# Kernel optimization log

Measured on AMD Instinct MI355X. Metric: run time of the kernel, lower is better.

The kernel has to match this reference:

```python
import jax, jax.numpy as jnp
import numpy as np

DIM = 256
NUM_HEADS = 4
HEAD_DIM = DIM // NUM_HEADS
SCALE = HEAD_DIM ** -0.5
LN_EPS = 1e-5


def setup_inputs() -> dict:
    key = jax.random.key(0)
    ks = jax.random.split(key, 12)
    V, B, C, H, W = 3, 2, DIM, 32, 32
    s = 0.02
    return {
        "features": jax.random.normal(ks[0], (V, B, C, H, W), jnp.float32),
        "Wq": jax.random.normal(ks[1], (DIM, DIM), jnp.float32) * s,
        "bq": jnp.zeros((DIM,), jnp.float32),
        "Wk": jax.random.normal(ks[2], (DIM, DIM), jnp.float32) * s,
        "bk": jnp.zeros((DIM,), jnp.float32),
        "Wv": jax.random.normal(ks[3], (DIM, DIM), jnp.float32) * s,
        "bv": jnp.zeros((DIM,), jnp.float32),
        "Wp": jax.random.normal(ks[4], (DIM, DIM), jnp.float32) * s,
        "bp": jnp.zeros((DIM,), jnp.float32),
        "gamma": jnp.ones((DIM,), jnp.float32),
        "beta": jnp.zeros((DIM,), jnp.float32),
    }


def reference(features, Wq, bq, Wk, bk, Wv, bv, Wp, bp, gamma, beta):
    V, B, C, H, W = features.shape
    N = H * W
    L = V * N
    # concat views along token axis: [B, V*N, C]
    x = features.reshape(V, B, C, N).transpose(1, 0, 3, 2).reshape(B, L, C)
    # QKV projections (torch Linear: x @ W.T + b)
    q = (x @ Wq.T + bq).reshape(B, L, NUM_HEADS, HEAD_DIM).transpose(0, 2, 1, 3)
    k = (x @ Wk.T + bk).reshape(B, L, NUM_HEADS, HEAD_DIM).transpose(0, 2, 1, 3)
    v = (x @ Wv.T + bv).reshape(B, L, NUM_HEADS, HEAD_DIM).transpose(0, 2, 1, 3)
    # full attention (chunked loop in original is exact, dropout off in eval)
    attn = jax.nn.softmax(jnp.einsum('bhqd,bhkd->bhqk', q, k) * SCALE, axis=-1)
    o = jnp.einsum('bhqk,bhkd->bhqd', attn, v)  # [B, H, L, D]
    o = o.transpose(0, 2, 1, 3).reshape(B, L, C)
    # output proj + LayerNorm
    o = o @ Wp.T + bp
    mu = jnp.mean(o, axis=-1, keepdims=True)
    var = jnp.mean(jnp.square(o - mu), axis=-1, keepdims=True)
    o = (o - mu) * jax.lax.rsqrt(var + LN_EPS) * gamma + beta
    # mean over views, back to [B, C, H, W]
    o = o.reshape(B, V, N, C).mean(axis=1)
    return o.reshape(B, H, W, C).transpose(0, 3, 1, 2)
```

## Files before the change

### kernel.cpp

```cpp
#include <hip/hip_runtime.h>
#include <hip/hip_bf16.h>

#define V_ 3
#define B_ 2
#define C_ 256
#define N_ 1024
#define L_ 3072
#define NH 4
#define DH 64
#define SCALE 0.125f
#define LOG2E 1.44269504088896340736f

typedef __attribute__((ext_vector_type(8))) short short8;
typedef __attribute__((ext_vector_type(4))) float floatx4;
typedef unsigned short u16;
typedef unsigned int u32;

__device__ __forceinline__ u16 f2bf(float f) {
    union { float f; u32 u; } c; c.f = f;
    u32 u = c.u;
    u32 lsb = (u >> 16) & 1u;
    u += 0x7fffu + lsb;
    return (u16)(u >> 16);
}
__device__ __forceinline__ u32 pk_bf16(float a, float b) {
    __hip_bfloat162 h = __float22bfloat162_rn(make_float2(a, b));
    union { __hip_bfloat162 h; u32 u; } cv; cv.h = h; return cv.u;
}

__global__ __launch_bounds__(256) void k_prep_gather(
    const float* __restrict__ feat,
    const float* __restrict__ Wq, const float* __restrict__ Wk,
    const float* __restrict__ Wv, const float* __restrict__ Wp,
    u16* __restrict__ x, u16* __restrict__ Wb) {
    int bid = blockIdx.x;
    int t = threadIdx.x;
    if (bid < 384) {
        __shared__ u16 tile[64][66];
        int n0 = (bid & 15) << 6;
        int c0 = ((bid >> 4) & 3) << 6;
        int b  = (bid >> 6) & 1;
        int v  = bid >> 7;
        const float* src = feat + ((size_t)((v * B_ + b) * C_ + c0)) * N_ + n0;
        for (int i = 0; i < 8; ++i) {
            int idx = i * 256 + t;
            int cl = idx >> 5;
            int np2 = idx & 31;
            float2 f = *(const float2*)(src + (size_t)cl * N_ + np2 * 2);
            *(u32*)&tile[cl][np2 * 2] = pk_bf16(f.x, f.y);
        }
        __syncthreads();
        u16* dst = x + ((size_t)(b * L_ + v * N_ + n0)) * C_ + c0;
        for (int i = 0; i < 8; ++i) {
            int idx = i * 256 + t;
            int nl = idx >> 5;
            int cl = (idx & 31) * 2;
            u32 uu = (u32)tile[cl][nl] | ((u32)tile[cl + 1][nl] << 16);
            *(u32*)(dst + (size_t)nl * C_ + cl) = uu;
        }
    } else {
        int idx = (bid - 384) * 256 + t;
        int g0 = idx * 16;
        int m = g0 >> 16;
        const float* src = (m == 0) ? Wq : (m == 1) ? Wk : (m == 2) ? Wv : Wp;
        int off = g0 & 65535;
#pragma unroll
        for (int e = 0; e < 8; ++e) {
            float2 f = *(const float2*)(src + off + e * 2);
            ((u32*)(Wb + g0))[e] = pk_bf16(f.x, f.y);
        }
    }
}


__global__ __launch_bounds__(64) void k_qkv(
    const u16* __restrict__ x, const u16* __restrict__ Wb,
    const float* __restrict__ bq, const float* __restrict__ bk,
    const float* __restrict__ bv,
    u16* __restrict__ Qf, u16* __restrict__ Kf, u16* __restrict__ Vf) {
    int bid = blockIdx.x;
    int npc = bid & 3;
    int rest = bid >> 2;
    int m  = rest / 192;
    int rb = rest % 192;
    int b  = rb / 96;
    int r0 = (rb % 96) * 32;
    int lane = threadIdx.x;
    int quad = lane >> 4, m16 = lane & 15;

    const u16* xrow0 = x + ((size_t)(b * L_ + r0 + m16)) * C_ + quad * 8;
    const u16* xrow1 = xrow0 + (size_t)16 * C_;
    short8 a0[8], a1[8];
#pragma unroll
    for (int kc = 0; kc < 8; ++kc) {
        a0[kc] = *(const short8*)(xrow0 + kc * 32);
        a1[kc] = *(const short8*)(xrow1 + kc * 32);
    }

    const u16* W   = Wb + (size_t)m * 65536;
    const float* bs = (m == 0) ? bq : (m == 1) ? bk : bv;
    float scale = (m == 0) ? (SCALE * LOG2E) : 1.0f;

#pragma unroll
    for (int np = npc * 2; np < npc * 2 + 2; ++np) {
        int nt0 = np * 2;
        const u16* w0 = W + (size_t)(nt0 * 16 + m16) * C_ + quad * 8;
        const u16* w1 = w0 + 16 * C_;
        short8 wf0[8], wf1[8];
#pragma unroll
        for (int kc = 0; kc < 8; ++kc) {
            wf0[kc] = *(const short8*)(w0 + kc * 32);
            wf1[kc] = *(const short8*)(w1 + kc * 32);
        }
        floatx4 acc00 = {0.f,0.f,0.f,0.f}, acc01 = {0.f,0.f,0.f,0.f};
        floatx4 acc10 = {0.f,0.f,0.f,0.f}, acc11 = {0.f,0.f,0.f,0.f};
#pragma unroll
        for (int kc = 0; kc < 8; ++kc) {
            acc00 = __builtin_amdgcn_mfma_f32_16x16x32_bf16(a0[kc], wf0[kc], acc00, 0, 0, 0);
            acc01 = __builtin_amdgcn_mfma_f32_16x16x32_bf16(a0[kc], wf1[kc], acc01, 0, 0, 0);
            acc10 = __builtin_amdgcn_mfma_f32_16x16x32_bf16(a1[kc], wf0[kc], acc10, 0, 0, 0);
            acc11 = __builtin_amdgcn_mfma_f32_16x16x32_bf16(a1[kc], wf1[kc], acc11, 0, 0, 0);
        }
#pragma unroll
        for (int gi = 0; gi < 2; ++gi)
#pragma unroll
        for (int half = 0; half < 2; ++half) {
            int dout = (nt0 + half) * 16 + m16;
            float bias = bs[dout];
            int h = dout >> 6, dh = dout & 63;
            size_t bh = (size_t)(b * NH + h);
            floatx4 acc = gi ? (half ? acc11 : acc10) : (half ? acc01 : acc00);
            float f0 = (acc[0] + bias) * scale, f1 = (acc[1] + bias) * scale;
            float f2 = (acc[2] + bias) * scale, f3 = (acc[3] + bias) * scale;
            int lr0 = r0 + gi * 16 + quad * 4;
            if (m == 2) {
                int tile = lr0 >> 6, kk = lr0 & 63;
                int halfv = kk >> 5, quadp = (kk >> 3) & 3, j0 = kk & 7;
                int ntv = dh >> 4, m16pp = dh & 15;
                u32* p = (u32*)(Vf + (bh * 48 + tile) * 4096 +
                                ((size_t)((ntv * 2 + halfv) * 64 + quadp * 16 + m16pp)) * 8 + j0);
                p[0] = pk_bf16(f0, f1);
                p[1] = pk_bf16(f2, f3);
            } else {
                int cc = dh >> 5, quadp = (dh >> 3) & 3, j = dh & 7;
                u32 p01 = pk_bf16(f0, f1);
                u32 p23 = pk_bf16(f2, f3);
                if (m == 0) {
#pragma unroll
                    for (int r = 0; r < 4; ++r) {
                        int lr = lr0 + r;
                        int grp = lr >> 4, m16p = lr & 15;
                        u32 pk = (r < 2) ? p01 : p23;
                        u16 val = (r & 1) ? (u16)(pk >> 16) : (u16)pk;
                        Qf[(bh * 192 + grp) * 1024 +
                           (size_t)(cc * 64 + quadp * 16 + m16p) * 8 + j] = val;
                    }
                } else {
#pragma unroll
                    for (int r = 0; r < 4; ++r) {
                        int lr = lr0 + r;
                        int tile = lr >> 6, rr = lr & 63;
                        int ntk = rr >> 4, m16p = rr & 15;
                        u32 pk = (r < 2) ? p01 : p23;
                        u16 val = (r & 1) ? (u16)(pk >> 16) : (u16)pk;
                        Kf[(bh * 48 + tile) * 4096 +
                           (size_t)((ntk * 2 + cc) * 64 + quadp * 16 + m16p) * 8 + j] = val;
                    }
                }
            }
        }
    }
}

__global__ __launch_bounds__(256, 2) void k_attn(
    const u16* __restrict__ Qf, const u16* __restrict__ Kf,
    const u16* __restrict__ Vf, u16* __restrict__ o) {
    __shared__ __align__(16) char smem[36864];
    __shared__ float l_red[3][3][16];
    u16* PL = (u16*)smem;
    float* o_red = (float*)smem;
    int bid = blockIdx.x;
    int qt = bid & 63;
    int h  = (bid >> 6) & 3;
    int b  = bid >> 8;
    int lane = threadIdx.x & 63;
    int w    = threadIdx.x >> 6;
    int quad = lane >> 4, m16 = lane & 15;
    int q0 = qt * 48;
    size_t bh = (size_t)(b * NH + h);

    const u16* qbase = Qf + (bh * 192 + qt * 3) * 1024 + (size_t)lane * 8;
    const u16* kbase = Kf + bh * 48 * 4096 + (size_t)lane * 8;
    const u16* vbase = Vf + bh * 48 * 4096 + (size_t)lane * 8;

    short8 aq[3][2];
#pragma unroll
    for (int g = 0; g < 3; ++g) {
        aq[g][0] = *(const short8*)(qbase + g * 1024);
        aq[g][1] = *(const short8*)(qbase + g * 1024 + 512);
    }

    float l_s[3] = {0.f, 0.f, 0.f};
    floatx4 o_acc[3][4];
#pragma unroll
    for (int g = 0; g < 3; ++g)
#pragma unroll
        for (int nt = 0; nt < 4; ++nt) o_acc[g][nt] = (floatx4){0.f, 0.f, 0.f, 0.f};

    int kt0 = w * 12;
    short8 kb[8], vb[8];
#pragma unroll
    for (int f = 0; f < 8; ++f)
        kb[f] = *(const short8*)(kbase + (size_t)kt0 * 4096 + f * 512);

    for (int i = 0; i < 12; ++i) {
        size_t tbase = (size_t)(kt0 + i) * 4096;
#pragma unroll
        for (int f = 0; f < 8; ++f)
            vb[f] = *(const short8*)(vbase + tbase + f * 512);
#pragma unroll
        for (int g = 0; g < 3; ++g) {
            floatx4 s[4];
#pragma unroll
            for (int nt = 0; nt < 4; ++nt) {
                floatx4 z = {0.f, 0.f, 0.f, 0.f};
                z = __builtin_amdgcn_mfma_f32_16x16x32_bf16(kb[nt * 2], aq[g][0], z, 0, 0, 0);
                s[nt] = __builtin_amdgcn_mfma_f32_16x16x32_bf16(kb[nt * 2 + 1], aq[g][1], z, 0, 0, 0);
            }
            u16* plrow = PL + (((w * 3 + g) * 16) + m16) * 72;
            float lsum = 0.f;
#pragma unroll
            for (int nt = 0; nt < 4; ++nt) {
                float p0 = __builtin_amdgcn_exp2f(s[nt][0]);
                float p1 = __builtin_amdgcn_exp2f(s[nt][1]);
                float p2 = __builtin_amdgcn_exp2f(s[nt][2]);
                float p3 = __builtin_amdgcn_exp2f(s[nt][3]);
                lsum += (p0 + p1) + (p2 + p3);
                uint2 pk; pk.x = pk_bf16(p0, p1); pk.y = pk_bf16(p2, p3);
                *(uint2*)(plrow + nt * 16 + quad * 4) = pk;
            }
            l_s[g] += lsum;
            short8 bp0 = *(const short8*)(plrow + quad * 8);
            short8 bp1 = *(const short8*)(plrow + 32 + quad * 8);
#pragma unroll
            for (int nt = 0; nt < 4; ++nt) {
                o_acc[g][nt] = __builtin_amdgcn_mfma_f32_16x16x32_bf16(vb[nt * 2], bp0, o_acc[g][nt], 0, 0, 0);
                o_acc[g][nt] = __builtin_amdgcn_mfma_f32_16x16x32_bf16(vb[nt * 2 + 1], bp1, o_acc[g][nt], 0, 0, 0);
            }
        }
        if (i < 11) {
#pragma unroll
            for (int f = 0; f < 8; ++f)
                kb[f] = *(const short8*)(kbase + tbase + 4096 + f * 512);
        }
    }
    float l_row[3];
#pragma unroll
    for (int g = 0; g < 3; ++g) {
        float ps = l_s[g];
        ps += __shfl_xor(ps, 16);
        ps += __shfl_xor(ps, 32);
        l_row[g] = ps;
    }
    __syncthreads();
    if (w > 0) {
#pragma unroll
        for (int g = 0; g < 3; ++g) {
#pragma unroll
            for (int nt = 0; nt < 4; ++nt)
                *(floatx4*)&o_red[(((w - 1) * 3 + g) * 4 + nt) * 256 + lane * 4] = o_acc[g][nt];
            if (quad == 0) l_red[w - 1][g][m16] = l_row[g];
        }
    }
    __syncthreads();
    if (w == 0) {
#pragma unroll
        for (int g = 0; g < 3; ++g) {
            float lt = __builtin_amdgcn_rcpf(
                l_row[g] + l_red[0][g][m16] + l_red[1][g][m16] + l_red[2][g][m16]);
#pragma unroll
            for (int nt = 0; nt < 4; ++nt) {
                floatx4 tot = o_acc[g][nt];
#pragma unroll
                for (int w1 = 0; w1 < 3; ++w1)
                    tot += *(const floatx4*)&o_red[((w1 * 3 + g) * 4 + nt) * 256 + lane * 4];
                uint2 pk;
                pk.x = pk_bf16(tot[0] * lt, tot[1] * lt);
                pk.y = pk_bf16(tot[2] * lt, tot[3] * lt);
                *(uint2*)(o + ((size_t)(b * L_ + q0 + g * 16 + m16)) * C_ +
                          h * 64 + nt * 16 + quad * 4) = pk;
            }
        }
    }
}

__global__ __launch_bounds__(256) void k_proj_ln(
    const u16* __restrict__ o, const u16* __restrict__ Wpb,
    const float* __restrict__ bp,
    const float* __restrict__ gamma, const float* __restrict__ beta,
    u16* __restrict__ oln) {
    __shared__ float sred[4][16];
    __shared__ float sred2[4][16];
    int bid = blockIdx.x;
    int n0 = (bid & 63) << 4;
    int b  = (bid >> 6) & 1;
    int v  = bid >> 7;
    int lane = threadIdx.x & 63;
    int w    = threadIdx.x >> 6;
    int quad = lane >> 4, m16 = lane & 15;

    const u16* orow = o + ((size_t)(b * L_ + v * N_ + n0 + m16)) * C_ + quad * 8;
    short8 a[8];
#pragma unroll
    for (int kc = 0; kc < 8; ++kc) a[kc] = *(const short8*)(orow + kc * 32);

    float pr[4][4];
#pragma unroll
    for (int j = 0; j < 4; ++j) {
        int nt = w * 4 + j;
        const u16* wrow = Wpb + (size_t)(nt * 16 + m16) * C_ + quad * 8;
        floatx4 acc = {0.f, 0.f, 0.f, 0.f};
#pragma unroll
        for (int kc = 0; kc < 8; ++kc) {
            short8 bfr = *(const short8*)(wrow + kc * 32);
            acc = __builtin_amdgcn_mfma_f32_16x16x32_bf16(a[kc], bfr, acc, 0, 0, 0);
        }
        float bias = bp[nt * 16 + m16];
#pragma unroll
        for (int r = 0; r < 4; ++r) pr[j][r] = acc[r] + bias;
    }
#pragma unroll
    for (int r = 0; r < 4; ++r) {
        float sm = pr[0][r] + pr[1][r] + pr[2][r] + pr[3][r];
        sm += __shfl_xor(sm, 1); sm += __shfl_xor(sm, 2);
        sm += __shfl_xor(sm, 4); sm += __shfl_xor(sm, 8);
        if (m16 == 0) sred[w][quad * 4 + r] = sm;
    }
    __syncthreads();
    float mu[4];
#pragma unroll
    for (int r = 0; r < 4; ++r) {
        int row = quad * 4 + r;
        mu[r] = (sred[0][row] + sred[1][row] + sred[2][row] + sred[3][row]) * (1.0f / C_);
    }
#pragma unroll
    for (int r = 0; r < 4; ++r) {
        float sq = 0.f;
#pragma unroll
        for (int j = 0; j < 4; ++j) { float d = pr[j][r] - mu[r]; sq += d * d; }
        sq += __shfl_xor(sq, 1); sq += __shfl_xor(sq, 2);
        sq += __shfl_xor(sq, 4); sq += __shfl_xor(sq, 8);
        if (m16 == 0) sred2[w][quad * 4 + r] = sq;
    }
    __syncthreads();
    float rs[4];
#pragma unroll
    for (int r = 0; r < 4; ++r) {
        int row = quad * 4 + r;
        float var = (sred2[0][row] + sred2[1][row] + sred2[2][row] + sred2[3][row]) * (1.0f / C_);
        rs[r] = __builtin_amdgcn_rsqf(var + 1e-5f);
    }
#pragma unroll
    for (int j = 0; j < 4; ++j) {
        int nt = w * 4 + j;
        int c = nt * 16 + m16;
        float g  = gamma[c];
        float be = beta[c];
#pragma unroll
        for (int r = 0; r < 4; ++r) {
            int row = quad * 4 + r;
            oln[((size_t)((v * B_ + b) * N_ + n0 + row)) * C_ + c] =
                f2bf((pr[j][r] - mu[r]) * rs[r] * g + be);
        }
    }
}

__global__ __launch_bounds__(256) void k_mean_t(
    const u16* __restrict__ oln, float* __restrict__ out) {
    __shared__ float tile[64][65];
    int bid = blockIdx.x;
    int n0 = (bid & 15) << 6;
    int c0 = ((bid >> 4) & 3) << 6;
    int b  = bid >> 6;
    int t = threadIdx.x;
    union { u32 u; float f; } cv;
    for (int i = 0; i < 16; ++i) {
        int idx = i * 256 + t;
        int nl = idx >> 6, cl = idx & 63;
        float sm = 0.f;
#pragma unroll
        for (int v = 0; v < 3; ++v) {
            u16 raw = oln[((size_t)((v * B_ + b) * N_ + n0 + nl)) * C_ + c0 + cl];
            cv.u = ((u32)raw) << 16;
            sm += cv.f;
        }
        tile[cl][nl] = sm * (1.0f / 3.0f);
    }
    __syncthreads();
    for (int i = 0; i < 16; ++i) {
        int idx = i * 256 + t;
        int cl = idx >> 6, nl = idx & 63;
        out[((size_t)(b * C_ + c0 + cl)) * N_ + n0 + nl] = tile[cl][nl];
    }
}

extern "C" void kernel_launch(void* const* d_in, const int* in_sizes, int n_in,
                              void* d_out, int out_size, void* d_ws, size_t ws_size,
                              hipStream_t stream) {
    (void)in_sizes; (void)n_in; (void)out_size; (void)ws_size;
    const float* feat  = (const float*)d_in[0];
    const float* Wq    = (const float*)d_in[1];
    const float* bq    = (const float*)d_in[2];
    const float* Wk    = (const float*)d_in[3];
    const float* bk    = (const float*)d_in[4];
    const float* Wv    = (const float*)d_in[5];
    const float* bv    = (const float*)d_in[6];
    const float* Wp    = (const float*)d_in[7];
    const float* bp    = (const float*)d_in[8];
    const float* gamma = (const float*)d_in[9];
    const float* beta  = (const float*)d_in[10];
    float* out = (float*)d_out;

    size_t SZ = (size_t)B_ * L_ * C_;
    u16* x   = (u16*)d_ws;
    u16* Qf  = x + SZ;
    u16* Kf  = Qf + SZ;
    u16* Vf  = Kf + SZ;
    u16* o   = Vf + SZ;
    u16* Wb  = o + SZ;
    u16* oln = Wb + 4 * 65536;

    k_prep_gather<<<dim3(448), dim3(256), 0, stream>>>(feat, Wq, Wk, Wv, Wp, x, Wb);
    k_qkv<<<dim3(2304), dim3(64), 0, stream>>>(x, Wb, bq, bk, bv, Qf, Kf, Vf);
    k_attn<<<dim3(512), dim3(256), 0, stream>>>(Qf, Kf, Vf, o);
    k_proj_ln<<<dim3(384), dim3(256), 0, stream>>>(o, Wb + 3 * 65536, bp, gamma, beta, oln);
    k_mean_t<<<dim3(128), dim3(256), 0, stream>>>(oln, out);
}
```

Measured before the change: 134.3 us.

## Split attention keys across two blocks, vectorize QKV and LN epilogue stores

The attention kernel is split along the key dimension into two halves, doubling the grid to 1024 blocks. Each block writes unnormalized fp32 partial outputs and row sums, and a new combine kernel adds them and normalizes. K and V fragments now share one register array to cut register pressure, and launch bounds target 3 blocks per CU. The Q/K projection and the proj+LayerNorm kernel swap MFMA operand order so each lane holds 4 consecutive channels, allowing vectorized bias loads and 8-byte stores instead of scattered 2-byte stores. The cost is an extra launch plus fp32 partial-result traffic.

```diff
diff --git a/kernel.cpp b/kernel.cpp
--- a/kernel.cpp
+++ b/kernel.cpp
@@ -72,7 +72,6 @@
     }
 }
 
-
 __global__ __launch_bounds__(64) void k_qkv(
     const u16* __restrict__ x, const u16* __restrict__ Wb,
     const float* __restrict__ bq, const float* __restrict__ bk,
@@ -96,44 +95,41 @@
         a0[kc] = *(const short8*)(xrow0 + kc * 32);
         a1[kc] = *(const short8*)(xrow1 + kc * 32);
     }
-
-    const u16* W   = Wb + (size_t)m * 65536;
-    const float* bs = (m == 0) ? bq : (m == 1) ? bk : bv;
-    float scale = (m == 0) ? (SCALE * LOG2E) : 1.0f;
-
-#pragma unroll
-    for (int np = npc * 2; np < npc * 2 + 2; ++np) {
-        int nt0 = np * 2;
-        const u16* w0 = W + (size_t)(nt0 * 16 + m16) * C_ + quad * 8;
-        const u16* w1 = w0 + 16 * C_;
-        short8 wf0[8], wf1[8];
-#pragma unroll
-        for (int kc = 0; kc < 8; ++kc) {
-            wf0[kc] = *(const short8*)(w0 + kc * 32);
-            wf1[kc] = *(const short8*)(w1 + kc * 32);
-        }
-        floatx4 acc00 = {0.f,0.f,0.f,0.f}, acc01 = {0.f,0.f,0.f,0.f};
-        floatx4 acc10 = {0.f,0.f,0.f,0.f}, acc11 = {0.f,0.f,0.f,0.f};
-#pragma unroll
-        for (int kc = 0; kc < 8; ++kc) {
-            acc00 = __builtin_amdgcn_mfma_f32_16x16x32_bf16(a0[kc], wf0[kc], acc00, 0, 0, 0);
-            acc01 = __builtin_amdgcn_mfma_f32_16x16x32_bf16(a0[kc], wf1[kc], acc01, 0, 0, 0);
-            acc10 = __builtin_amdgcn_mfma_f32_16x16x32_bf16(a1[kc], wf0[kc], acc10, 0, 0, 0);
-            acc11 = __builtin_amdgcn_mfma_f32_16x16x32_bf16(a1[kc], wf1[kc], acc11, 0, 0, 0);
-        }
-#pragma unroll
-        for (int gi = 0; gi < 2; ++gi)
-#pragma unroll
-        for (int half = 0; half < 2; ++half) {
-            int dout = (nt0 + half) * 16 + m16;
-            float bias = bs[dout];
-            int h = dout >> 6, dh = dout & 63;
-            size_t bh = (size_t)(b * NH + h);
-            floatx4 acc = gi ? (half ? acc11 : acc10) : (half ? acc01 : acc00);
-            float f0 = (acc[0] + bias) * scale, f1 = (acc[1] + bias) * scale;
-            float f2 = (acc[2] + bias) * scale, f3 = (acc[3] + bias) * scale;
-            int lr0 = r0 + gi * 16 + quad * 4;
-            if (m == 2) {
+    const u16* W = Wb + (size_t)m * 65536;
+
+    if (m == 2) {
+#pragma unroll
+        for (int np = npc * 2; np < npc * 2 + 2; ++np) {
+            int nt0 = np * 2;
+            const u16* w0 = W + (size_t)(nt0 * 16 + m16) * C_ + quad * 8;
+            const u16* w1 = w0 + 16 * C_;
+            short8 wf0[8], wf1[8];
+#pragma unroll
+            for (int kc = 0; kc < 8; ++kc) {
+                wf0[kc] = *(const short8*)(w0 + kc * 32);
+                wf1[kc] = *(const short8*)(w1 + kc * 32);
+            }
+            floatx4 acc00 = {0.f,0.f,0.f,0.f}, acc01 = {0.f,0.f,0.f,0.f};
+            floatx4 acc10 = {0.f,0.f,0.f,0.f}, acc11 = {0.f,0.f,0.f,0.f};
+#pragma unroll
+            for (int kc = 0; kc < 8; ++kc) {
+                acc00 = __builtin_amdgcn_mfma_f32_16x16x32_bf16(a0[kc], wf0[kc], acc00, 0, 0, 0);
+                acc01 = __builtin_amdgcn_mfma_f32_16x16x32_bf16(a0[kc], wf1[kc], acc01, 0, 0, 0);
+                acc10 = __builtin_amdgcn_mfma_f32_16x16x32_bf16(a1[kc], wf0[kc], acc10, 0, 0, 0);
+                acc11 = __builtin_amdgcn_mfma_f32_16x16x32_bf16(a1[kc], wf1[kc], acc11, 0, 0, 0);
+            }
+#pragma unroll
+            for (int gi = 0; gi < 2; ++gi)
+#pragma unroll
+            for (int half = 0; half < 2; ++half) {
+                int dout = (nt0 + half) * 16 + m16;
+                float bias = bv[dout];
+                int h = dout >> 6, dh = dout & 63;
+                size_t bh = (size_t)(b * NH + h);
+                floatx4 acc = gi ? (half ? acc11 : acc10) : (half ? acc01 : acc00);
+                float f0 = acc[0] + bias, f1 = acc[1] + bias;
+                float f2 = acc[2] + bias, f3 = acc[3] + bias;
+                int lr0 = r0 + gi * 16 + quad * 4;
                 int tile = lr0 >> 6, kk = lr0 & 63;
                 int halfv = kk >> 5, quadp = (kk >> 3) & 3, j0 = kk & 7;
                 int ntv = dh >> 4, m16pp = dh & 15;
@@ -141,52 +137,79 @@
                                 ((size_t)((ntv * 2 + halfv) * 64 + quadp * 16 + m16pp)) * 8 + j0);
                 p[0] = pk_bf16(f0, f1);
                 p[1] = pk_bf16(f2, f3);
-            } else {
-                int cc = dh >> 5, quadp = (dh >> 3) & 3, j = dh & 7;
-                u32 p01 = pk_bf16(f0, f1);
-                u32 p23 = pk_bf16(f2, f3);
+            }
+        }
+    } else {
+        const float* bs = (m == 0) ? bq : bk;
+        float scale = (m == 0) ? (SCALE * LOG2E) : 1.0f;
+#pragma unroll
+        for (int np = npc * 2; np < npc * 2 + 2; ++np) {
+            int nt0 = np * 2;
+            const u16* w0 = W + (size_t)(nt0 * 16 + m16) * C_ + quad * 8;
+            const u16* w1 = w0 + 16 * C_;
+            short8 wf0[8], wf1[8];
+#pragma unroll
+            for (int kc = 0; kc < 8; ++kc) {
+                wf0[kc] = *(const short8*)(w0 + kc * 32);
+                wf1[kc] = *(const short8*)(w1 + kc * 32);
+            }
+            floatx4 acc00 = {0.f,0.f,0.f,0.f}, acc01 = {0.f,0.f,0.f,0.f};
+            floatx4 acc10 = {0.f,0.f,0.f,0.f}, acc11 = {0.f,0.f,0.f,0.f};
+#pragma unroll
+            for (int kc = 0; kc < 8; ++kc) {
+                acc00 = __builtin_amdgcn_mfma_f32_16x16x32_bf16(wf0[kc], a0[kc], acc00, 0, 0, 0);
+                acc01 = __builtin_amdgcn_mfma_f32_16x16x32_bf16(wf0[kc], a1[kc], acc01, 0, 0, 0);
+                acc10 = __builtin_amdgcn_mfma_f32_16x16x32_bf16(wf1[kc], a0[kc], acc10, 0, 0, 0);
+                acc11 = __builtin_amdgcn_mfma_f32_16x16x32_bf16(wf1[kc], a1[kc], acc11, 0, 0, 0);
+            }
+#pragma unroll
+            for (int tt = 0; tt < 2; ++tt)
+#pragma unroll
+            for (int gi = 0; gi < 2; ++gi) {
+                int ntb = (nt0 + tt) * 16;
+                int h = ntb >> 6;
+                size_t bh = (size_t)(b * NH + h);
+                int dh0 = (ntb & 63) + quad * 4;
+                int cc = dh0 >> 5, qp = (dh0 >> 3) & 3, j0 = dh0 & 7;
+                float4 b4 = *(const float4*)(bs + ntb + quad * 4);
+                floatx4 acc = tt ? (gi ? acc11 : acc10) : (gi ? acc01 : acc00);
+                float f0 = (acc[0] + b4.x) * scale, f1 = (acc[1] + b4.y) * scale;
+                float f2 = (acc[2] + b4.z) * scale, f3 = (acc[3] + b4.w) * scale;
+                uint2 pk;
+                pk.x = pk_bf16(f0, f1);
+                pk.y = pk_bf16(f2, f3);
+                int token = r0 + gi * 16 + m16;
                 if (m == 0) {
-#pragma unroll
-                    for (int r = 0; r < 4; ++r) {
-                        int lr = lr0 + r;
-                        int grp = lr >> 4, m16p = lr & 15;
-                        u32 pk = (r < 2) ? p01 : p23;
-                        u16 val = (r & 1) ? (u16)(pk >> 16) : (u16)pk;
-                        Qf[(bh * 192 + grp) * 1024 +
-                           (size_t)(cc * 64 + quadp * 16 + m16p) * 8 + j] = val;
-                    }
+                    int grp = (r0 >> 4) + gi;
+                    *(uint2*)(Qf + (bh * 192 + grp) * 1024 +
+                              (size_t)(cc * 64 + qp * 16 + m16) * 8 + j0) = pk;
                 } else {
-#pragma unroll
-                    for (int r = 0; r < 4; ++r) {
-                        int lr = lr0 + r;
-                        int tile = lr >> 6, rr = lr & 63;
-                        int ntk = rr >> 4, m16p = rr & 15;
-                        u32 pk = (r < 2) ? p01 : p23;
-                        u16 val = (r & 1) ? (u16)(pk >> 16) : (u16)pk;
-                        Kf[(bh * 48 + tile) * 4096 +
-                           (size_t)((ntk * 2 + cc) * 64 + quadp * 16 + m16p) * 8 + j] = val;
-                    }
+                    int tile = token >> 6;
+                    int ntk = ((r0 & 63) >> 4) + gi;
+                    *(uint2*)(Kf + (bh * 48 + tile) * 4096 +
+                              (size_t)((ntk * 2 + cc) * 64 + qp * 16 + m16) * 8 + j0) = pk;
                 }
             }
         }
     }
 }
 
-__global__ __launch_bounds__(256, 2) void k_attn(
+__global__ __launch_bounds__(256, 3) void k_attn(
     const u16* __restrict__ Qf, const u16* __restrict__ Kf,
-    const u16* __restrict__ Vf, u16* __restrict__ o) {
+    const u16* __restrict__ Vf, float* __restrict__ o_p, float* __restrict__ l_p) {
     __shared__ __align__(16) char smem[36864];
     __shared__ float l_red[3][3][16];
     u16* PL = (u16*)smem;
     float* o_red = (float*)smem;
     int bid = blockIdx.x;
-    int qt = bid & 63;
-    int h  = (bid >> 6) & 3;
-    int b  = bid >> 8;
+    int rest = bid & 511;
+    int s  = bid >> 9;
+    int qt = rest & 63;
+    int h  = (rest >> 6) & 3;
+    int b  = rest >> 8;
     int lane = threadIdx.x & 63;
     int w    = threadIdx.x >> 6;
     int quad = lane >> 4, m16 = lane & 15;
-    int q0 = qt * 48;
     size_t bh = (size_t)(b * NH + h);
 
     const u16* qbase = Qf + (bh * 192 + qt * 3) * 1024 + (size_t)lane * 8;
@@ -207,51 +230,50 @@
 #pragma unroll
         for (int nt = 0; nt < 4; ++nt) o_acc[g][nt] = (floatx4){0.f, 0.f, 0.f, 0.f};
 
-    int kt0 = w * 12;
-    short8 kb[8], vb[8];
-#pragma unroll
-    for (int f = 0; f < 8; ++f)
-        kb[f] = *(const short8*)(kbase + (size_t)kt0 * 4096 + f * 512);
-
-    for (int i = 0; i < 12; ++i) {
+    int kt0 = s * 24 + w * 6;
+    short8 kv[8];
+
+    for (int i = 0; i < 6; ++i) {
         size_t tbase = (size_t)(kt0 + i) * 4096;
 #pragma unroll
         for (int f = 0; f < 8; ++f)
-            vb[f] = *(const short8*)(vbase + tbase + f * 512);
+            kv[f] = *(const short8*)(kbase + tbase + f * 512);
 #pragma unroll
         for (int g = 0; g < 3; ++g) {
-            floatx4 s[4];
+            floatx4 sx[4];
 #pragma unroll
             for (int nt = 0; nt < 4; ++nt) {
                 floatx4 z = {0.f, 0.f, 0.f, 0.f};
-                z = __builtin_amdgcn_mfma_f32_16x16x32_bf16(kb[nt * 2], aq[g][0], z, 0, 0, 0);
-                s[nt] = __builtin_amdgcn_mfma_f32_16x16x32_bf16(kb[nt * 2 + 1], aq[g][1], z, 0, 0, 0);
+                z = __builtin_amdgcn_mfma_f32_16x16x32_bf16(kv[nt * 2], aq[g][0], z, 0, 0, 0);
+                sx[nt] = __builtin_amdgcn_mfma_f32_16x16x32_bf16(kv[nt * 2 + 1], aq[g][1], z, 0, 0, 0);
             }
             u16* plrow = PL + (((w * 3 + g) * 16) + m16) * 72;
             float lsum = 0.f;
 #pragma unroll
             for (int nt = 0; nt < 4; ++nt) {
-                float p0 = __builtin_amdgcn_exp2f(s[nt][0]);
-                float p1 = __builtin_amdgcn_exp2f(s[nt][1]);
-                float p2 = __builtin_amdgcn_exp2f(s[nt][2]);
-                float p3 = __builtin_amdgcn_exp2f(s[nt][3]);
+                float p0 = __builtin_amdgcn_exp2f(sx[nt][0]);
+                float p1 = __builtin_amdgcn_exp2f(sx[nt][1]);
+                float p2 = __builtin_amdgcn_exp2f(sx[nt][2]);
+                float p3 = __builtin_amdgcn_exp2f(sx[nt][3]);
                 lsum += (p0 + p1) + (p2 + p3);
                 uint2 pk; pk.x = pk_bf16(p0, p1); pk.y = pk_bf16(p2, p3);
                 *(uint2*)(plrow + nt * 16 + quad * 4) = pk;
             }
             l_s[g] += lsum;
+        }
+#pragma unroll
+        for (int f = 0; f < 8; ++f)
+            kv[f] = *(const short8*)(vbase + tbase + f * 512);
+#pragma unroll
+        for (int g = 0; g < 3; ++g) {
+            const u16* plrow = PL + (((w * 3 + g) * 16) + m16) * 72;
             short8 bp0 = *(const short8*)(plrow + quad * 8);
             short8 bp1 = *(const short8*)(plrow + 32 + quad * 8);
 #pragma unroll
             for (int nt = 0; nt < 4; ++nt) {
-                o_acc[g][nt] = __builtin_amdgcn_mfma_f32_16x16x32_bf16(vb[nt * 2], bp0, o_acc[g][nt], 0, 0, 0);
-                o_acc[g][nt] = __builtin_amdgcn_mfma_f32_16x16x32_bf16(vb[nt * 2 + 1], bp1, o_acc[g][nt], 0, 0, 0);
-            }
-        }
-        if (i < 11) {
-#pragma unroll
-            for (int f = 0; f < 8; ++f)
-                kb[f] = *(const short8*)(kbase + tbase + 4096 + f * 512);
+                o_acc[g][nt] = __builtin_amdgcn_mfma_f32_16x16x32_bf16(kv[nt * 2], bp0, o_acc[g][nt], 0, 0, 0);
+                o_acc[g][nt] = __builtin_amdgcn_mfma_f32_16x16x32_bf16(kv[nt * 2 + 1], bp1, o_acc[g][nt], 0, 0, 0);
+            }
         }
     }
     float l_row[3];
@@ -276,21 +298,44 @@
     if (w == 0) {
 #pragma unroll
         for (int g = 0; g < 3; ++g) {
-            float lt = __builtin_amdgcn_rcpf(
-                l_row[g] + l_red[0][g][m16] + l_red[1][g][m16] + l_red[2][g][m16]);
+            if (quad == 0)
+                l_p[(size_t)bid * 48 + g * 16 + m16] =
+                    l_row[g] + l_red[0][g][m16] + l_red[1][g][m16] + l_red[2][g][m16];
 #pragma unroll
             for (int nt = 0; nt < 4; ++nt) {
                 floatx4 tot = o_acc[g][nt];
 #pragma unroll
                 for (int w1 = 0; w1 < 3; ++w1)
                     tot += *(const floatx4*)&o_red[((w1 * 3 + g) * 4 + nt) * 256 + lane * 4];
-                uint2 pk;
-                pk.x = pk_bf16(tot[0] * lt, tot[1] * lt);
-                pk.y = pk_bf16(tot[2] * lt, tot[3] * lt);
-                *(uint2*)(o + ((size_t)(b * L_ + q0 + g * 16 + m16)) * C_ +
-                          h * 64 + nt * 16 + quad * 4) = pk;
-            }
-        }
+                *(floatx4*)&o_p[(((size_t)bid * 3 + g) * 4 + nt) * 256 + lane * 4] = tot;
+            }
+        }
+    }
+}
+
+__global__ __launch_bounds__(192) void k_comb(
+    const float* __restrict__ o_p, const float* __restrict__ l_p,
+    u16* __restrict__ o) {
+    int bid = blockIdx.x;
+    int qt = bid & 63;
+    int h  = (bid >> 6) & 3;
+    int b  = bid >> 8;
+    int lane = threadIdx.x & 63;
+    int g    = threadIdx.x >> 6;
+    int quad = lane >> 4, m16 = lane & 15;
+    float l = l_p[(size_t)bid * 48 + g * 16 + m16] +
+              l_p[(size_t)(bid + 512) * 48 + g * 16 + m16];
+    float lt = __builtin_amdgcn_rcpf(l);
+#pragma unroll
+    for (int nt = 0; nt < 4; ++nt) {
+        floatx4 t0 = *(const floatx4*)&o_p[(((size_t)bid * 3 + g) * 4 + nt) * 256 + lane * 4];
+        floatx4 t1 = *(const floatx4*)&o_p[(((size_t)(bid + 512) * 3 + g) * 4 + nt) * 256 + lane * 4];
+        floatx4 tot = t0 + t1;
+        uint2 pk;
+        pk.x = pk_bf16(tot[0] * lt, tot[1] * lt);
+        pk.y = pk_bf16(tot[2] * lt, tot[3] * lt);
+        *(uint2*)(o + ((size_t)(b * L_ + qt * 48 + g * 16 + m16)) * C_ +
+                  h * 64 + nt * 16 + quad * 4) = pk;
     }
 }
 
@@ -323,55 +368,45 @@
 #pragma unroll
         for (int kc = 0; kc < 8; ++kc) {
             short8 bfr = *(const short8*)(wrow + kc * 32);
-            acc = __builtin_amdgcn_mfma_f32_16x16x32_bf16(a[kc], bfr, acc, 0, 0, 0);
-        }
-        float bias = bp[nt * 16 + m16];
-#pragma unroll
-        for (int r = 0; r < 4; ++r) pr[j][r] = acc[r] + bias;
-    }
-#pragma unroll
-    for (int r = 0; r < 4; ++r) {
-        float sm = pr[0][r] + pr[1][r] + pr[2][r] + pr[3][r];
-        sm += __shfl_xor(sm, 1); sm += __shfl_xor(sm, 2);
-        sm += __shfl_xor(sm, 4); sm += __shfl_xor(sm, 8);
-        if (m16 == 0) sred[w][quad * 4 + r] = sm;
-    }
+            acc = __builtin_amdgcn_mfma_f32_16x16x32_bf16(bfr, a[kc], acc, 0, 0, 0);
+        }
+        float4 b4 = *(const float4*)(bp + nt * 16 + quad * 4);
+        pr[j][0] = acc[0] + b4.x; pr[j][1] = acc[1] + b4.y;
+        pr[j][2] = acc[2] + b4.z; pr[j][3] = acc[3] + b4.w;
+    }
+    float sm = 0.f;
+#pragma unroll
+    for (int j = 0; j < 4; ++j)
+        sm += (pr[j][0] + pr[j][1]) + (pr[j][2] + pr[j][3]);
+    sm += __shfl_xor(sm, 16);
+    sm += __shfl_xor(sm, 32);
+    if (quad == 0) sred[w][m16] = sm;
     __syncthreads();
-    float mu[4];
-#pragma unroll
-    for (int r = 0; r < 4; ++r) {
-        int row = quad * 4 + r;
-        mu[r] = (sred[0][row] + sred[1][row] + sred[2][row] + sred[3][row]) * (1.0f / C_);
-    }
-#pragma unroll
-    for (int r = 0; r < 4; ++r) {
-        float sq = 0.f;
-#pragma unroll
-        for (int j = 0; j < 4; ++j) { float d = pr[j][r] - mu[r]; sq += d * d; }
-        sq += __shfl_xor(sq, 1); sq += __shfl_xor(sq, 2);
-        sq += __shfl_xor(sq, 4); sq += __shfl_xor(sq, 8);
-        if (m16 == 0) sred2[w][quad * 4 + r] = sq;
-    }
+    float mu = (sred[0][m16] + sred[1][m16] + sred[2][m16] + sred[3][m16]) * (1.0f / C_);
+    float sq = 0.f;
+#pragma unroll
+    for (int j = 0; j < 4; ++j)
+#pragma unroll
+        for (int r = 0; r < 4; ++r) { float d = pr[j][r] - mu; sq += d * d; }
+    sq += __shfl_xor(sq, 16);
+    sq += __shfl_xor(sq, 32);
+    if (quad == 0) sred2[w][m16] = sq;
     __syncthreads();
-    float rs[4];
-#pragma unroll
-    for (int r = 0; r < 4; ++r) {
-        int row = quad * 4 + r;
-        float var = (sred2[0][row] + sred2[1][row] + sred2[2][row] + sred2[3][row]) * (1.0f / C_);
-        rs[r] = __builtin_amdgcn_rsqf(var + 1e-5f);
-    }
+    float var = (sred2[0][m16] + sred2[1][m16] + sred2[2][m16] + sred2[3][m16]) * (1.0f / C_);
+    float rs = __builtin_amdgcn_rsqf(var + 1e-5f);
 #pragma unroll
     for (int j = 0; j < 4; ++j) {
-        int nt = w * 4 + j;
-        int c = nt * 16 + m16;
-        float g  = gamma[c];
-        float be = beta[c];
-#pragma unroll
-        for (int r = 0; r < 4; ++r) {
-            int row = quad * 4 + r;
-            oln[((size_t)((v * B_ + b) * N_ + n0 + row)) * C_ + c] =
-                f2bf((pr[j][r] - mu[r]) * rs[r] * g + be);
-        }
+        int c0 = (w * 4 + j) * 16 + quad * 4;
+        float4 g4 = *(const float4*)(gamma + c0);
+        float4 be4 = *(const float4*)(beta + c0);
+        float f0 = (pr[j][0] - mu) * rs * g4.x + be4.x;
+        float f1 = (pr[j][1] - mu) * rs * g4.y + be4.y;
+        float f2 = (pr[j][2] - mu) * rs * g4.z + be4.z;
+        float f3 = (pr[j][3] - mu) * rs * g4.w + be4.w;
+        uint2 pk;
+        pk.x = pk_bf16(f0, f1);
+        pk.y = pk_bf16(f2, f3);
+        *(uint2*)(oln + ((size_t)((v * B_ + b) * N_ + n0 + m16)) * C_ + c0) = pk;
     }
 }
 
@@ -429,10 +464,13 @@
     u16* o   = Vf + SZ;
     u16* Wb  = o + SZ;
     u16* oln = Wb + 4 * 65536;
+    float* o_p = (float*)(oln + SZ);
+    float* l_p = o_p + (size_t)1024 * 3072;
 
     k_prep_gather<<<dim3(448), dim3(256), 0, stream>>>(feat, Wq, Wk, Wv, Wp, x, Wb);
     k_qkv<<<dim3(2304), dim3(64), 0, stream>>>(x, Wb, bq, bk, bv, Qf, Kf, Vf);
-    k_attn<<<dim3(512), dim3(256), 0, stream>>>(Qf, Kf, Vf, o);
+    k_attn<<<dim3(1024), dim3(256), 0, stream>>>(Qf, Kf, Vf, o_p, l_p);
+    k_comb<<<dim3(512), dim3(192), 0, stream>>>(o_p, l_p, o);
     k_proj_ln<<<dim3(384), dim3(256), 0, stream>>>(o, Wb + 3 * 65536, bp, gamma, beta, oln);
     k_mean_t<<<dim3(128), dim3(256), 0, stream>>>(oln, out);
 }
```

After: 140.5 us. +4.6%, slower.
